# Optimization experiments

Measured on AMD Instinct MI355X. Metric: run time of the kernel, lower is better.

Reference implementation:

```python
import jax, jax.numpy as jnp
import numpy as np

PATCH = 16
ATT_DEPTH = 2
DOWN = 2 ** ATT_DEPTH  # 4


def _unfold(x, p):
    # torch nn.Unfold(kernel=p, stride=p) on (B, C, H, W) single-channel slices,
    # vectorized over C. Returns (B, C, p*p, L) with L = (H//p)*(W//p),
    # kernel elements in row-major order, patches in row-major order (matches torch).
    B, C, H, W = x.shape
    xr = x.reshape(B, C, H // p, p, W // p, p)
    xr = xr.transpose(0, 1, 3, 5, 2, 4)  # (B, C, p, p, H//p, W//p)
    return xr.reshape(B, C, p * p, (H // p) * (W // p))


def setup_inputs() -> dict:
    key = jax.random.key(0)
    k1, k2, k3 = jax.random.split(key, 3)
    B, C, H, W = 8, 4, 1024, 1024
    L = (H // PATCH) * (W // PATCH)            # 4096
    L2 = (H // DOWN // PATCH) * (W // DOWN // PATCH)  # 256
    pred = jax.random.normal(k1, (B, C, H, W), dtype=jnp.float32)
    target = jax.random.randint(k2, (B, H, W), 0, C, dtype=jnp.int64)
    attentions = jax.random.uniform(k3, (B, C, L, L2), dtype=jnp.float32)
    return {"pred": pred, "target": target, "attentions": attentions}


def reference(pred, target, attentions):
    B, C, H, W = pred.shape
    # activation (softmax over class dim); pred is not used further in the loss,
    # kept for faithfulness to the original forward.
    _ = jax.nn.softmax(pred, axis=1)
    # one-hot ground truth, (B, C, H, W) float32
    y_gt = (target[:, None, :, :] == jnp.arange(C, dtype=target.dtype)[None, :, None, None]).astype(jnp.float32)
    # grouped conv with all-ones 4x4 kernel, stride 4, divided by 16 == 4x4 average pool
    y_gt_conv = y_gt.reshape(B, C, H // DOWN, DOWN, W // DOWN, DOWN).mean(axis=(3, 5))
    # unfold both maps: (B, C, p*p, L) and (B, C, p*p, L2)
    u_gt = _unfold(y_gt, PATCH)
    u_conv = _unfold(y_gt_conv, PATCH)
    # att[b,c,l,m] = sum_k u_gt[b,c,k,l] * u_conv[b,c,k,m] / p^2
    attentions_gt = jnp.einsum('bckl,bckm->bclm', u_gt, u_conv) / float(PATCH * PATCH)
    # MSE (mean reduction)
    return jnp.mean((attentions - attentions_gt) ** 2)
```

## Files before the change

### kernel.cpp

```cpp
#include <hip/hip_runtime.h>
#include <stdint.h>


#define BDIM 256

typedef int v4i  __attribute__((ext_vector_type(4)));
typedef int v16i __attribute__((ext_vector_type(16)));

__global__ __launch_bounds__(BDIM) void cls_kernel(
    const int* __restrict__ tgt, uint8_t* __restrict__ cls,
    float* __restrict__ dout) {
  int id = blockIdx.x * BDIM + threadIdx.x;
  if (id == 0) *dout = 0.f;
  int b  = id >> 16;
  int l  = (id >> 4) & 4095;
  int ky = id & 15;
  int h  = ((l >> 6) << 4) + ky;
  int w  = (l & 63) << 4;
  const int* p = tgt + ((size_t)b << 20) + ((size_t)h << 10) + w;
  uint32_t o[4];
#pragma unroll
  for (int i = 0; i < 4; ++i) {
    int4 v = *(const int4*)(p + (i << 2));
    o[i] = (uint32_t)v.x | ((uint32_t)v.y << 8) |
           ((uint32_t)v.z << 16) | ((uint32_t)v.w << 24);
  }
  *(uint4*)(cls + ((size_t)b << 20) + ((size_t)l << 8) + (ky << 4)) =
      make_uint4(o[0], o[1], o[2], o[3]);
}

__global__ __launch_bounds__(BDIM) void cnt_kernel(
    const uint8_t* __restrict__ cls, uint8_t* __restrict__ cntT) {
  int id = blockIdx.x * BDIM + threadIdx.x;
  int b = id >> 16;
  int Y = (id >> 8) & 255;
  int X = id & 255;
  int l = ((Y >> 2) << 6) | (X >> 2);
  const uint8_t* p = cls + ((size_t)b << 20) + ((size_t)l << 8) +
                     ((Y & 3) << 6) + ((X & 3) << 2);
  uint32_t pc = 0;
#pragma unroll
  for (int dy = 0; dy < 4; ++dy) {
    uint32_t wv = *(const uint32_t*)(p + (dy << 4));
#pragma unroll
    for (int s = 0; s < 32; s += 8)
      pc += 1u << (((wv >> s) & 3u) << 3);
  }
  int m  = ((Y >> 4) << 4) | (X >> 4);
  int km = ((Y & 15) << 4) | (X & 15);
  size_t o = ((size_t)b << 18) | ((size_t)m << 8) | (size_t)km;
#pragma unroll
  for (int c = 0; c < 4; ++c)
    cntT[o + ((size_t)c << 16)] = (uint8_t)((pc >> (c << 3)) & 0xFFu);
}

__global__ __launch_bounds__(BDIM) void gemm_kernel(
    const uint8_t* __restrict__ cls, const uint8_t* __restrict__ cntT,
    const float* __restrict__ att, float* __restrict__ dout) {
  __shared__ float wsum[4];
  const int t    = threadIdx.x;
  const int wv   = t >> 6, lane = t & 63;
  const int bc   = blockIdx.y;
  const int b    = bc >> 2, c = bc & 3;
  const int l0   = (blockIdx.x << 7) + (wv << 5);
  const int lrow  = lane & 31;
  const int khalf = lane >> 5;

  const uint32_t crep = (uint32_t)c * 0x01010101u;
  v4i afr[8];
  const uint8_t* abase = cls + ((size_t)b << 20) +
                         ((size_t)(l0 + lrow) << 8) + (khalf << 4);
#pragma unroll
  for (int kk = 0; kk < 8; ++kk) {
    uint4 raw = *(const uint4*)(abase + (kk << 5));
    uint32_t r[4] = {raw.x, raw.y, raw.z, raw.w};
    v4i a;
#pragma unroll
    for (int i = 0; i < 4; ++i) {
      uint32_t x = r[i] ^ crep;
      uint32_t nz = (x | (x >> 1)) & 0x01010101u;
      a[i] = (int)(nz ^ 0x01010101u);
    }
    afr[kk] = a;
  }

  const uint8_t* bbase = cntT + ((size_t)bc << 16) + (khalf << 4);
  const float* attbase = att + ((size_t)bc << 20) +
                         ((size_t)(l0 + (khalf << 2)) << 8) + lrow;
  float lsum = 0.f;

#pragma unroll 1
  for (int mc = 0; mc < 8; ++mc) {
    const float* ap = attbase + (mc << 5);
    float av[16];
#pragma unroll
    for (int reg = 0; reg < 16; ++reg)
      av[reg] = ap[((reg & 3) << 8) + ((reg >> 2) << 11)];

    v16i acc = {0,0,0,0,0,0,0,0,0,0,0,0,0,0,0,0};
    const uint8_t* bb = bbase + ((size_t)((mc << 5) + lrow) << 8);
#pragma unroll
    for (int kk = 0; kk < 8; ++kk) {
      uint4 raw = *(const uint4*)(bb + (kk << 5));
      v4i bfr;
      bfr[0] = (int)raw.x; bfr[1] = (int)raw.y;
      bfr[2] = (int)raw.z; bfr[3] = (int)raw.w;
      acc = __builtin_amdgcn_mfma_i32_32x32x32_i8(afr[kk], bfr, acc, 0, 0, 0);
    }
#pragma unroll
    for (int reg = 0; reg < 16; ++reg) {
      float d = fmaf((float)acc[reg], -1.f / 4096.f, av[reg]);
      lsum = fmaf(d, d, lsum);
    }
  }

#pragma unroll
  for (int o = 32; o > 0; o >>= 1) lsum += __shfl_down(lsum, o, 64);
  if (lane == 0) wsum[wv] = lsum;
  __syncthreads();
  if (t == 0) {
    float s = (wsum[0] + wsum[1]) + (wsum[2] + wsum[3]);
    atomicAdd(dout, s * (1.f / 33554432.f));
  }
}

extern "C" void kernel_launch(void* const* d_in, const int* in_sizes, int n_in,
                              void* d_out, int out_size, void* d_ws, size_t ws_size,
                              hipStream_t stream) {
  (void)in_sizes; (void)n_in; (void)out_size; (void)ws_size;
  const int*   tgt = (const int*)d_in[1];
  const float* att = (const float*)d_in[2];
  float* dout      = (float*)d_out;
  uint8_t* cls     = (uint8_t*)d_ws;
  uint8_t* cntT    = (uint8_t*)d_ws + (8u << 20);

  cls_kernel<<<dim3(524288 / BDIM), BDIM, 0, stream>>>(tgt, cls, dout);
  cnt_kernel<<<dim3(524288 / BDIM), BDIM, 0, stream>>>(cls, cntT);
  gemm_kernel<<<dim3(32, 32), BDIM, 0, stream>>>(cls, cntT, att, dout);
}
```

Baseline: 282.3 us.

## Fuse class-packing and pooled-count kernels into one LDS-staged prep kernel

Merges cls_kernel and cnt_kernel into a single prep_kernel. Each block loads a 16x256 target tile into shared memory, writes the packed class bytes, and computes the 4x4 pooled counts straight from shared memory. This removes one launch and the global re-read of the cls buffer, and it makes global target reads row-contiguous. In exchange it adds a __syncthreads per block, possible LDS bank conflicts, and 2048 blocks instead of 2x2048.

```diff
diff --git a/kernel.cpp b/kernel.cpp
--- a/kernel.cpp
+++ b/kernel.cpp
@@ -7,51 +7,57 @@
 typedef int v4i  __attribute__((ext_vector_type(4)));
 typedef int v16i __attribute__((ext_vector_type(16)));
 
-__global__ __launch_bounds__(BDIM) void cls_kernel(
+__global__ __launch_bounds__(BDIM) void prep_kernel(
     const int* __restrict__ tgt, uint8_t* __restrict__ cls,
-    float* __restrict__ dout) {
-  int id = blockIdx.x * BDIM + threadIdx.x;
-  if (id == 0) *dout = 0.f;
-  int b  = id >> 16;
-  int l  = (id >> 4) & 4095;
-  int ky = id & 15;
-  int h  = ((l >> 6) << 4) + ky;
-  int w  = (l & 63) << 4;
-  const int* p = tgt + ((size_t)b << 20) + ((size_t)h << 10) + w;
-  uint32_t o[4];
+    uint8_t* __restrict__ cntT, float* __restrict__ dout) {
+  __shared__ uint4 lcls[16][17];
+  const int t   = threadIdx.x;
+  const int blk = blockIdx.x;
+  if (blk == 0 && t == 0) *dout = 0.f;
+  const int b  = blk >> 8;
+  const int hr = (blk >> 2) & 63;
+  const int wq = blk & 3;
+
+  {
+    const int row = t >> 4, wb = t & 15;
+    const int* p = tgt + ((size_t)b << 20) + ((size_t)((hr << 4) + row) << 10)
+                 + (wq << 8) + (wb << 4);
+    uint32_t o[4];
 #pragma unroll
-  for (int i = 0; i < 4; ++i) {
-    int4 v = *(const int4*)(p + (i << 2));
-    o[i] = (uint32_t)v.x | ((uint32_t)v.y << 8) |
-           ((uint32_t)v.z << 16) | ((uint32_t)v.w << 24);
+    for (int i = 0; i < 4; ++i) {
+      int4 v = *(const int4*)(p + (i << 2));
+      o[i] = (uint32_t)v.x | ((uint32_t)v.y << 8) |
+             ((uint32_t)v.z << 16) | ((uint32_t)v.w << 24);
+    }
+    lcls[row][wb] = make_uint4(o[0], o[1], o[2], o[3]);
   }
-  *(uint4*)(cls + ((size_t)b << 20) + ((size_t)l << 8) + (ky << 4)) =
-      make_uint4(o[0], o[1], o[2], o[3]);
-}
+  __syncthreads();
 
-__global__ __launch_bounds__(BDIM) void cnt_kernel(
-    const uint8_t* __restrict__ cls, uint8_t* __restrict__ cntT) {
-  int id = blockIdx.x * BDIM + threadIdx.x;
-  int b = id >> 16;
-  int Y = (id >> 8) & 255;
-  int X = id & 255;
-  int l = ((Y >> 2) << 6) | (X >> 2);
-  const uint8_t* p = cls + ((size_t)b << 20) + ((size_t)l << 8) +
-                     ((Y & 3) << 6) + ((X & 3) << 2);
-  uint32_t pc = 0;
+  {
+    const int wb = t >> 4, ky = t & 15;
+    const int l = (hr << 6) + (wq << 4) + wb;
+    *(uint4*)(cls + ((size_t)b << 20) + ((size_t)l << 8) + (ky << 4)) =
+        lcls[ky][wb];
+  }
+
+  {
+    const int py = t >> 6, px = t & 63;
+    uint32_t pc = 0;
 #pragma unroll
-  for (int dy = 0; dy < 4; ++dy) {
-    uint32_t wv = *(const uint32_t*)(p + (dy << 4));
+    for (int dy = 0; dy < 4; ++dy) {
+      uint32_t wv = ((const uint32_t*)&lcls[(py << 2) + dy][px >> 2])[px & 3];
 #pragma unroll
-    for (int s = 0; s < 32; s += 8)
-      pc += 1u << (((wv >> s) & 3u) << 3);
+      for (int s = 0; s < 32; s += 8)
+        pc += 1u << (((wv >> s) & 3u) << 3);
+    }
+    const int Y = (hr << 2) + py, X = (wq << 6) + px;
+    const int m  = ((Y >> 4) << 4) | (X >> 4);
+    const int km = ((Y & 15) << 4) | (X & 15);
+    size_t o = ((size_t)b << 18) | ((size_t)m << 8) | (size_t)km;
+#pragma unroll
+    for (int c = 0; c < 4; ++c)
+      cntT[o + ((size_t)c << 16)] = (uint8_t)((pc >> (c << 3)) & 0xFFu);
   }
-  int m  = ((Y >> 4) << 4) | (X >> 4);
-  int km = ((Y & 15) << 4) | (X & 15);
-  size_t o = ((size_t)b << 18) | ((size_t)m << 8) | (size_t)km;
-#pragma unroll
-  for (int c = 0; c < 4; ++c)
-    cntT[o + ((size_t)c << 16)] = (uint8_t)((pc >> (c << 3)) & 0xFFu);
 }
 
 __global__ __launch_bounds__(BDIM) void gemm_kernel(
@@ -134,7 +140,6 @@
   uint8_t* cls     = (uint8_t*)d_ws;
   uint8_t* cntT    = (uint8_t*)d_ws + (8u << 20);
 
-  cls_kernel<<<dim3(524288 / BDIM), BDIM, 0, stream>>>(tgt, cls, dout);
-  cnt_kernel<<<dim3(524288 / BDIM), BDIM, 0, stream>>>(cls, cntT);
+  prep_kernel<<<dim3(2048), BDIM, 0, stream>>>(tgt, cls, cntT, dout);
   gemm_kernel<<<dim3(32, 32), BDIM, 0, stream>>>(cls, cntT, att, dout);
 }
```

After: 279.0 us. About the same (-1.2%).
